# Performance work log

Hardware: AMD Instinct MI355X
Metric: run time of the kernel (lower is better)

Reference implementation:

```python
import jax, jax.numpy as jnp
import numpy as np

DIM = 64
HID = DIM // 8  # 8, hidden width of pos_fc / attn_fc
B, N, V = 1024, 64, 8
NUM_IDS = 10


def setup_inputs() -> dict:
    key = jax.random.key(0)
    ks = jax.random.split(key, 24)
    stdv = 1.0 / np.sqrt(DIM * DIM)
    inp = {
        "q": jax.random.normal(ks[0], (B, N, DIM), jnp.float32),
        "k": jax.random.normal(ks[1], (B, N, V, DIM), jnp.float32),
        "pos": jax.random.normal(ks[2], (B, N, V, 4), jnp.float32),
        "strength": jax.random.normal(ks[3], (512,), jnp.float32),
        # learned params
        "q_tbl": jax.random.uniform(ks[4], (NUM_IDS, DIM * DIM), jnp.float32, -stdv, stdv),
        "k_tbl": jax.random.uniform(ks[5], (NUM_IDS, DIM * DIM), jnp.float32, -stdv, stdv),
        "v_tbl": jax.random.uniform(ks[6], (NUM_IDS, DIM * DIM), jnp.float32, -stdv, stdv),
        "pos_w1": jax.random.normal(ks[7], (4, HID), jnp.float32) * 0.5,
        "pos_b1": jax.random.normal(ks[8], (HID,), jnp.float32) * 0.1,
        "pos_w2": jax.random.normal(ks[9], (HID, DIM), jnp.float32) * 0.2,
        "pos_b2": jax.random.normal(ks[10], (DIM,), jnp.float32) * 0.1,
        "attn_w1": jax.random.normal(ks[11], (DIM, HID), jnp.float32) * 0.1,
        "attn_b1": jax.random.normal(ks[12], (HID,), jnp.float32) * 0.1,
        "attn_w2": jax.random.normal(ks[13], (HID, DIM), jnp.float32) * 0.2,
        "attn_b2": jax.random.normal(ks[14], (DIM,), jnp.float32) * 0.1,
        "out_w": jax.random.normal(ks[15], (DIM, DIM), jnp.float32) * 0.1,
        "out_b": jax.random.normal(ks[16], (DIM,), jnp.float32) * 0.1,
        "str_w": jax.random.normal(ks[17], (512, DIM), jnp.float32) * 0.04,
        "str_b": jax.random.normal(ks[18], (DIM,), jnp.float32) * 0.1,
        # int args
        "mask": jax.random.randint(ks[19], (B, N, V, 1), 0, 2, jnp.int32),
        "embed_id1": 3,
    }
    return inp


def reference(q, k, pos, strength, q_tbl, k_tbl, v_tbl,
              pos_w1, pos_b1, pos_w2, pos_b2,
              attn_w1, attn_b1, attn_w2, attn_b2,
              out_w, out_b, str_w, str_b, mask, embed_id1):
    s = strength @ str_w + str_b                       # [DIM]
    Wq = q_tbl[embed_id1].reshape(DIM, DIM)
    Wk = k_tbl[embed_id1].reshape(DIM, DIM)
    Wv = v_tbl[embed_id1].reshape(DIM, DIM)
    # F.linear(x, W) = x @ W.T ; note v is computed from k (as in source)
    qh = q @ Wq.T + s                                  # [B,N,DIM]
    kh = k @ Wk.T + s                                  # [B,N,V,DIM]
    vh = k @ Wv.T + s                                  # [B,N,V,DIM]
    p = jax.nn.relu(pos @ pos_w1 + pos_b1) @ pos_w2 + pos_b2   # [B,N,V,DIM]
    attn = kh - qh[:, :, None, :] + p                  # [B,N,V,DIM]
    attn = jax.nn.relu(attn @ attn_w1 + attn_b1) @ attn_w2 + attn_b2
    attn = jnp.where(mask == 0, jnp.float32(-1e9), attn)
    attn = jax.nn.softmax(attn, axis=-2)               # softmax over views V
    x = ((vh + p) * attn).sum(axis=2)                  # [B,N,DIM]
    x = x @ out_w + out_b
    return x
```

## Files before the change

kernel.cpp:

```cpp
#include <hip/hip_runtime.h>

#define TBL 4096

#define WS_SPB 0
#define WS_C0  64
#define WS_IMG 128
#define IMG_BH  0
#define IMG_BCT 4
#define IMG_BP  5
#define IMG_BW2 9
#define IMG_BV  13
#define IMG_BO  21

typedef __attribute__((ext_vector_type(8))) short bf16x8;
typedef __attribute__((ext_vector_type(4))) float f32x4;

__device__ inline int cvt2bf(float a, float b) {
    int r;
    asm("v_cvt_pk_bf16_f32 %0, %1, %2" : "=v"(r) : "v"(a), "v"(b));
    return r;
}

__device__ inline bf16x8 pack8(const float* x) {
    union { int4 i; bf16x8 b; } u;
    u.i.x = cvt2bf(x[0], x[1]);
    u.i.y = cvt2bf(x[2], x[3]);
    u.i.z = cvt2bf(x[4], x[5]);
    u.i.w = cvt2bf(x[6], x[7]);
    return u.b;
}

__device__ inline bf16x8 loadpack(const float* p) {
    float4 a = *(const float4*)p;
    float4 b = *(const float4*)(p + 4);
    float t[8] = {a.x, a.y, a.z, a.w, b.x, b.y, b.z, b.w};
    return pack8(t);
}

__device__ inline float swz16(float x) {
    return __int_as_float(__builtin_amdgcn_ds_swizzle(__float_as_int(x), 0x401F));
}

__global__ __launch_bounds__(256) void precompute_kernel(
    const float* __restrict__ strength, const float* __restrict__ str_w,
    const float* __restrict__ str_b,
    const float* __restrict__ q_tbl, const float* __restrict__ k_tbl,
    const float* __restrict__ v_tbl, const float* __restrict__ out_w,
    const float* __restrict__ attn_w1, const float* __restrict__ attn_b1,
    const float* __restrict__ attn_w2,
    const float* __restrict__ pos_w2, const float* __restrict__ pos_b2,
    const int* __restrict__ embed_id, float* __restrict__ ws)
{
    __shared__ float red[4][64];
    __shared__ float red2[4][64][8];

    const int t    = threadIdx.x;
    const int b    = blockIdx.x;
    const int id   = embed_id[0];
    const int lane = t & 63;
    const int dp   = t >> 6;
    const int q4   = lane >> 4;
    const int col  = lane & 15;

    if (b == 0) {
        {
            const float* st = strength + dp * 128;
            const float* sw = str_w + (size_t)(dp * 128) * 64 + lane;
            float a0 = 0.f, a1 = 0.f, a2 = 0.f, a3 = 0.f;
            #pragma unroll
            for (int i = 0; i < 128; i += 4) {
                a0 += st[i]     * sw[(size_t)(i)     * 64];
                a1 += st[i + 1] * sw[(size_t)(i + 1) * 64];
                a2 += st[i + 2] * sw[(size_t)(i + 2) * 64];
                a3 += st[i + 3] * sw[(size_t)(i + 3) * 64];
            }
            red[dp][lane] = (a0 + a1) + (a2 + a3);
        }
        if (t < 8) {
            float c = attn_b1[t];
            #pragma unroll
            for (int d = 0; d < 64; ++d) c += pos_b2[d] * attn_w1[d * 8 + t];
            ws[WS_C0 + t] = c;
        }
        __syncthreads();
        if (t < 64)
            ws[WS_SPB + t] = red[0][t] + red[1][t] + red[2][t] + red[3][t]
                           + str_b[t] + pos_b2[t];
        return;
    }

    const int im = b - 1;

    if (im < 5) {
        float val[8];
        #pragma unroll
        for (int j = 0; j < 8; ++j) val[j] = 0.f;

        if (im < 4) {
            const float* tbl = (im < 2 ? k_tbl : q_tbl) + (size_t)id * TBL;
            const int kb = (im & 1) * 32 + q4 * 8;
            if (col < 8) {
                #pragma unroll
                for (int dd = 0; dd < 16; ++dd) {
                    const int d = dp * 16 + dd;
                    const float w = attn_w1[d * 8 + col];
                    const float4 t0 = *(const float4*)(tbl + d * 64 + kb);
                    const float4 t1 = *(const float4*)(tbl + d * 64 + kb + 4);
                    val[0] += t0.x * w; val[1] += t0.y * w;
                    val[2] += t0.z * w; val[3] += t0.w * w;
                    val[4] += t1.x * w; val[5] += t1.y * w;
                    val[6] += t1.z * w; val[7] += t1.w * w;
                }
            }
        } else {
            if (q4 == 0 && col < 8) {
                #pragma unroll
                for (int dd = 0; dd < 16; ++dd) {
                    const int d = dp * 16 + dd;
                    const float w = attn_w1[d * 8 + col];
                    #pragma unroll
                    for (int j = 0; j < 8; ++j) val[j] += pos_w2[j * 64 + d] * w;
                }
            }
        }
        #pragma unroll
        for (int j = 0; j < 8; ++j) red2[dp][lane][j] = val[j];
        __syncthreads();
        if (dp == 0) {
            const float sgn = (im == 2 || im == 3) ? -1.f : 1.f;
            float v2[8];
            #pragma unroll
            for (int j = 0; j < 8; ++j)
                v2[j] = sgn * (red2[0][lane][j] + red2[1][lane][j] +
                               red2[2][lane][j] + red2[3][lane][j]);
            ((bf16x8*)(ws + WS_IMG))[im * 64 + lane] = pack8(v2);
        }
        return;
    }

    if (dp == 0) {
        float val[8];
        #pragma unroll
        for (int j = 0; j < 8; ++j) val[j] = 0.f;

        if (im < 9) {
            const int tt = im - 5;
            if (q4 == 0) {
                #pragma unroll
                for (int j = 0; j < 8; ++j) val[j] = pos_w2[j * 64 + tt * 16 + col];
            }
        } else if (im < 13) {
            const int tt = im - 9;
            if (q4 == 0) {
                #pragma unroll
                for (int j = 0; j < 8; ++j) val[j] = attn_w2[j * 64 + tt * 16 + col];
            }
        } else if (im < 21) {
            const int e = im - 13, tt = e >> 1, c = e & 1;
            const float* p = v_tbl + (size_t)id * TBL +
                             (tt * 16 + col) * 64 + c * 32 + q4 * 8;
            const float4 t0 = *(const float4*)p;
            const float4 t1 = *(const float4*)(p + 4);
            val[0] = t0.x; val[1] = t0.y; val[2] = t0.z; val[3] = t0.w;
            val[4] = t1.x; val[5] = t1.y; val[6] = t1.z; val[7] = t1.w;
        } else {
            const int e = im - 21, tt = e >> 1, c = e & 1;
            #pragma unroll
            for (int j = 0; j < 8; ++j)
                val[j] = out_w[(c * 32 + q4 * 8 + j) * 64 + tt * 16 + col];
        }
        ((bf16x8*)(ws + WS_IMG))[im * 64 + lane] = pack8(val);
    }
}

__global__ __launch_bounds__(256, 4) void attn2d_main(
    const float* __restrict__ q, const float* __restrict__ k,
    const float* __restrict__ pos,
    const float* __restrict__ pos_w1, const float* __restrict__ pos_b1,
    const float* __restrict__ attn_b2, const float* __restrict__ out_b,
    const int* __restrict__ mask,
    const float* __restrict__ ws, float* __restrict__ out)
{
    __shared__ float rh_lds[4][16 * 12];
    __shared__ float x_lds[4][8 * 68];

    const int tid  = threadIdx.x;
    const int lane = tid & 63;
    const int wiv  = __builtin_amdgcn_readfirstlane(tid >> 6);
    const int q4   = lane >> 4;
    const int col  = lane & 15;

    float* rh_w = rh_lds[wiv];
    float* x_w  = x_lds[wiv];

    const int wid = blockIdx.x * 4 + wiv;
    const bf16x8* img = (const bf16x8*)(ws + WS_IMG);

    bf16x8 Bh[4];
    #pragma unroll
    for (int c = 0; c < 4; ++c) Bh[c] = img[(IMG_BH + c) * 64 + lane];
    const bf16x8 Bct = img[IMG_BCT * 64 + lane];

    float spb[4], b2a[4];
    #pragma unroll
    for (int t = 0; t < 4; ++t) {
        spb[t] = ws[WS_SPB + t * 16 + col];
        b2a[t] = attn_b2[t * 16 + col];
    }
    const float c0r = (col < 8) ? ws[WS_C0 + col] : 0.f;
    const int bnp = q4 >> 1;

    #pragma unroll
    for (int it = 0; it < 4; ++it) {
        const int pair = wid * 4 + it;
        const int bn0  = pair * 2;

        bf16x8 Ak[2], Aq[2];
        #pragma unroll
        for (int c = 0; c < 2; ++c)
            Ak[c] = loadpack(k + ((size_t)pair * 16 + col) * 64 + c * 32 + q4 * 8);
        #pragma unroll
        for (int c = 0; c < 2; ++c)
            Aq[c] = loadpack(q + (size_t)(bn0 + (col >> 3)) * 64 + c * 32 + q4 * 8);

        const int4 m4v = *(const int4*)(mask + (size_t)pair * 16 + q4 * 4);
        const int mm[4] = {m4v.x, m4v.y, m4v.z, m4v.w};

        bf16x8 Ahp{};
        if (lane < 16) {
            float4 pp = *(const float4*)(pos + ((size_t)pair * 16 + lane) * 4);
            float hv[8];
            #pragma unroll
            for (int g = 0; g < 8; ++g)
                hv[g] = fmaxf(pos_b1[g] + pp.x * pos_w1[g] + pp.y * pos_w1[8 + g] +
                              pp.z * pos_w1[16 + g] + pp.w * pos_w1[24 + g], 0.f);
            Ahp = pack8(hv);
        }

        f32x4 acch = {0.f, 0.f, 0.f, 0.f};
        acch = __builtin_amdgcn_mfma_f32_16x16x32_bf16(Ak[0], Bh[0], acch, 0, 0, 0);
        acch = __builtin_amdgcn_mfma_f32_16x16x32_bf16(Ak[1], Bh[1], acch, 0, 0, 0);
        acch = __builtin_amdgcn_mfma_f32_16x16x32_bf16(Aq[0], Bh[2], acch, 0, 0, 0);
        acch = __builtin_amdgcn_mfma_f32_16x16x32_bf16(Aq[1], Bh[3], acch, 0, 0, 0);
        acch = __builtin_amdgcn_mfma_f32_16x16x32_bf16(Ahp,   Bct,   acch, 0, 0, 0);
        if (col < 8) {
            #pragma unroll
            for (int r = 0; r < 4; ++r)
                rh_w[(q4 * 4 + r) * 12 + col] = fmaxf(acch[r] + c0r, 0.f);
        }

        bf16x8 Arh{};
        if (q4 == 0) {
            float4 a  = *(const float4*)&rh_w[col * 12];
            float4 bb = *(const float4*)&rh_w[col * 12 + 4];
            float rr[8] = {a.x, a.y, a.z, a.w, bb.x, bb.y, bb.z, bb.w};
            Arh = pack8(rr);
        }

        #pragma unroll
        for (int t = 0; t < 4; ++t) {
            const bf16x8 Bv0 = img[(IMG_BV + t * 2) * 64 + lane];
            const bf16x8 Bv1 = img[(IMG_BV + t * 2 + 1) * 64 + lane];
            const bf16x8 Bp  = img[(IMG_BP + t) * 64 + lane];
            const bf16x8 Bw  = img[(IMG_BW2 + t) * 64 + lane];

            f32x4 vh = {0.f, 0.f, 0.f, 0.f};
            vh = __builtin_amdgcn_mfma_f32_16x16x32_bf16(Ak[0], Bv0, vh, 0, 0, 0);
            vh = __builtin_amdgcn_mfma_f32_16x16x32_bf16(Ak[1], Bv1, vh, 0, 0, 0);
            vh = __builtin_amdgcn_mfma_f32_16x16x32_bf16(Ahp,   Bp,  vh, 0, 0, 0);
            f32x4 at = {0.f, 0.f, 0.f, 0.f};
            at = __builtin_amdgcn_mfma_f32_16x16x32_bf16(Arh, Bw, at, 0, 0, 0);

            float lg[4];
            #pragma unroll
            for (int r = 0; r < 4; ++r)
                lg[r] = (mm[r] != 0) ? (at[r] + b2a[t]) : -1e9f;

            float mx = fmaxf(fmaxf(lg[0], lg[1]), fmaxf(lg[2], lg[3]));
            mx = fmaxf(mx, swz16(mx));
            float wsum = 0.f, xp = 0.f;
            #pragma unroll
            for (int r = 0; r < 4; ++r) {
                const float wv = __expf(lg[r] - mx);
                wsum += wv;
                xp   += wv * (vh[r] + spb[t]);
            }
            wsum += swz16(wsum);
            xp   += swz16(xp);
            const float xv = xp * __builtin_amdgcn_rcpf(wsum);
            if ((q4 & 1) == 0)
                x_w[(it * 2 + bnp) * 68 + t * 16 + col] = xv;
        }
    }

    bf16x8 Ax[2];
    #pragma unroll
    for (int c = 0; c < 2; ++c)
        Ax[c] = loadpack(&x_w[(col & 7) * 68 + c * 32 + q4 * 8]);
    #pragma unroll
    for (int t = 0; t < 4; ++t) {
        const bf16x8 Bo0 = img[(IMG_BO + t * 2) * 64 + lane];
        const bf16x8 Bo1 = img[(IMG_BO + t * 2 + 1) * 64 + lane];
        f32x4 a = {0.f, 0.f, 0.f, 0.f};
        a = __builtin_amdgcn_mfma_f32_16x16x32_bf16(Ax[0], Bo0, a, 0, 0, 0);
        a = __builtin_amdgcn_mfma_f32_16x16x32_bf16(Ax[1], Bo1, a, 0, 0, 0);
        const float ob = out_b[t * 16 + col];
        #pragma unroll
        for (int r = 0; r < 4; ++r) {
            const int row = q4 * 4 + r;
            if (row < 8)
                out[((size_t)wid * 8 + row) * 64 + t * 16 + col] = a[r] + ob;
        }
    }
}

extern "C" void kernel_launch(void* const* d_in, const int* in_sizes, int n_in,
                              void* d_out, int out_size, void* d_ws, size_t ws_size,
                              hipStream_t stream) {
    const float* q        = (const float*)d_in[0];
    const float* k        = (const float*)d_in[1];
    const float* pos      = (const float*)d_in[2];
    const float* strength = (const float*)d_in[3];
    const float* q_tbl    = (const float*)d_in[4];
    const float* k_tbl    = (const float*)d_in[5];
    const float* v_tbl    = (const float*)d_in[6];
    const float* pos_w1   = (const float*)d_in[7];
    const float* pos_b1   = (const float*)d_in[8];
    const float* pos_w2   = (const float*)d_in[9];
    const float* pos_b2   = (const float*)d_in[10];
    const float* attn_w1  = (const float*)d_in[11];
    const float* attn_b1  = (const float*)d_in[12];
    const float* attn_w2  = (const float*)d_in[13];
    const float* attn_b2  = (const float*)d_in[14];
    const float* out_w    = (const float*)d_in[15];
    const float* out_b    = (const float*)d_in[16];
    const float* str_w    = (const float*)d_in[17];
    const float* str_b    = (const float*)d_in[18];
    const int*   mask     = (const int*)d_in[19];
    const int*   embed    = (const int*)d_in[20];
    float* ws  = (float*)d_ws;
    float* out = (float*)d_out;

    hipLaunchKernelGGL(precompute_kernel, dim3(30), dim3(256), 0, stream,
                       strength, str_w, str_b, q_tbl, k_tbl, v_tbl, out_w,
                       attn_w1, attn_b1, attn_w2, pos_w2, pos_b2, embed, ws);
    hipLaunchKernelGGL(attn2d_main, dim3(2048), dim3(256), 0, stream,
                       q, k, pos, pos_w1, pos_b1, attn_b2, out_b, mask, ws, out);
}
```

Before: 270.2 us.

## Software-pipeline k/q/pos/mask loads and hoist weight fragments into registers

Prefetches the raw k, q, pos and mask data for the next pair while the current pair's MFMAs and softmax run, double-buffering them in registers. The per-tile B-fragment loads for V, pos, attn_w2 and out_w are hoisted out of the inner loops into registers. Launch bounds drop from 4 to 3 waves-per-EU occupancy to make room for the extra registers. This is meant to hide global memory latency, at the cost of lower occupancy.

```diff
diff --git a/kernel.cpp b/kernel.cpp
--- a/kernel.cpp
+++ b/kernel.cpp
@@ -30,11 +30,15 @@
     return u.b;
 }
 
+__device__ inline bf16x8 pack2f4(float4 a, float4 b) {
+    float t[8] = {a.x, a.y, a.z, a.w, b.x, b.y, b.z, b.w};
+    return pack8(t);
+}
+
 __device__ inline bf16x8 loadpack(const float* p) {
     float4 a = *(const float4*)p;
     float4 b = *(const float4*)(p + 4);
-    float t[8] = {a.x, a.y, a.z, a.w, b.x, b.y, b.z, b.w};
-    return pack8(t);
+    return pack2f4(a, b);
 }
 
 __device__ inline float swz16(float x) {
@@ -173,7 +177,7 @@
     }
 }
 
-__global__ __launch_bounds__(256, 4) void attn2d_main(
+__global__ __launch_bounds__(256, 3) void attn2d_main(
     const float* __restrict__ q, const float* __restrict__ k,
     const float* __restrict__ pos,
     const float* __restrict__ pos_w1, const float* __restrict__ pos_b1,
@@ -200,6 +204,14 @@
     #pragma unroll
     for (int c = 0; c < 4; ++c) Bh[c] = img[(IMG_BH + c) * 64 + lane];
     const bf16x8 Bct = img[IMG_BCT * 64 + lane];
+    bf16x8 Bv[4][2], Bp[4], Bw[4];
+    #pragma unroll
+    for (int t = 0; t < 4; ++t) {
+        Bv[t][0] = img[(IMG_BV + t * 2) * 64 + lane];
+        Bv[t][1] = img[(IMG_BV + t * 2 + 1) * 64 + lane];
+        Bp[t]    = img[(IMG_BP + t) * 64 + lane];
+        Bw[t]    = img[(IMG_BW2 + t) * 64 + lane];
+    }
 
     float spb[4], b2a[4];
     #pragma unroll
@@ -210,32 +222,50 @@
     const float c0r = (col < 8) ? ws[WS_C0 + col] : 0.f;
     const int bnp = q4 >> 1;
 
+#define LOADRAW(PAIR, RK, RQ, RP, RM) do {                                    \
+        const size_t kb_ = ((size_t)(PAIR) * 16 + col) * 64 + q4 * 8;         \
+        RK[0] = *(const float4*)(k + kb_);                                    \
+        RK[1] = *(const float4*)(k + kb_ + 4);                                \
+        RK[2] = *(const float4*)(k + kb_ + 32);                               \
+        RK[3] = *(const float4*)(k + kb_ + 36);                               \
+        const size_t qb_ = ((size_t)(PAIR) * 2 + (col >> 3)) * 64 + q4 * 8;   \
+        RQ[0] = *(const float4*)(q + qb_);                                    \
+        RQ[1] = *(const float4*)(q + qb_ + 4);                                \
+        RQ[2] = *(const float4*)(q + qb_ + 32);                               \
+        RQ[3] = *(const float4*)(q + qb_ + 36);                               \
+        if (lane < 16)                                                        \
+            RP = *(const float4*)(pos + ((size_t)(PAIR) * 16 + lane) * 4);    \
+        RM = *(const int4*)(mask + (size_t)(PAIR) * 16 + q4 * 4);             \
+    } while (0)
+
+    float4 rk[4], rq[4], rp = make_float4(0.f, 0.f, 0.f, 0.f);
+    int4   rm = make_int4(1, 1, 1, 1);
+    LOADRAW(wid * 4, rk, rq, rp, rm);
+
     #pragma unroll
     for (int it = 0; it < 4; ++it) {
         const int pair = wid * 4 + it;
-        const int bn0  = pair * 2;
 
         bf16x8 Ak[2], Aq[2];
-        #pragma unroll
-        for (int c = 0; c < 2; ++c)
-            Ak[c] = loadpack(k + ((size_t)pair * 16 + col) * 64 + c * 32 + q4 * 8);
-        #pragma unroll
-        for (int c = 0; c < 2; ++c)
-            Aq[c] = loadpack(q + (size_t)(bn0 + (col >> 3)) * 64 + c * 32 + q4 * 8);
-
-        const int4 m4v = *(const int4*)(mask + (size_t)pair * 16 + q4 * 4);
-        const int mm[4] = {m4v.x, m4v.y, m4v.z, m4v.w};
+        Ak[0] = pack2f4(rk[0], rk[1]);
+        Ak[1] = pack2f4(rk[2], rk[3]);
+        Aq[0] = pack2f4(rq[0], rq[1]);
+        Aq[1] = pack2f4(rq[2], rq[3]);
+        const int mm[4] = {rm.x, rm.y, rm.z, rm.w};
 
         bf16x8 Ahp{};
         if (lane < 16) {
-            float4 pp = *(const float4*)(pos + ((size_t)pair * 16 + lane) * 4);
             float hv[8];
             #pragma unroll
             for (int g = 0; g < 8; ++g)
-                hv[g] = fmaxf(pos_b1[g] + pp.x * pos_w1[g] + pp.y * pos_w1[8 + g] +
-                              pp.z * pos_w1[16 + g] + pp.w * pos_w1[24 + g], 0.f);
+                hv[g] = fmaxf(pos_b1[g] + rp.x * pos_w1[g] + rp.y * pos_w1[8 + g] +
+                              rp.z * pos_w1[16 + g] + rp.w * pos_w1[24 + g], 0.f);
             Ahp = pack8(hv);
         }
+
+        float4 nk[4], nq[4], np = make_float4(0.f, 0.f, 0.f, 0.f);
+        int4   nm = make_int4(1, 1, 1, 1);
+        if (it < 3) LOADRAW(pair + 1, nk, nq, np, nm);
 
         f32x4 acch = {0.f, 0.f, 0.f, 0.f};
         acch = __builtin_amdgcn_mfma_f32_16x16x32_bf16(Ak[0], Bh[0], acch, 0, 0, 0);
@@ -253,23 +283,17 @@
         if (q4 == 0) {
             float4 a  = *(const float4*)&rh_w[col * 12];
             float4 bb = *(const float4*)&rh_w[col * 12 + 4];
-            float rr[8] = {a.x, a.y, a.z, a.w, bb.x, bb.y, bb.z, bb.w};
-            Arh = pack8(rr);
+            Arh = pack2f4(a, bb);
         }
 
         #pragma unroll
         for (int t = 0; t < 4; ++t) {
-            const bf16x8 Bv0 = img[(IMG_BV + t * 2) * 64 + lane];
-            const bf16x8 Bv1 = img[(IMG_BV + t * 2 + 1) * 64 + lane];
-            const bf16x8 Bp  = img[(IMG_BP + t) * 64 + lane];
-            const bf16x8 Bw  = img[(IMG_BW2 + t) * 64 + lane];
-
             f32x4 vh = {0.f, 0.f, 0.f, 0.f};
-            vh = __builtin_amdgcn_mfma_f32_16x16x32_bf16(Ak[0], Bv0, vh, 0, 0, 0);
-            vh = __builtin_amdgcn_mfma_f32_16x16x32_bf16(Ak[1], Bv1, vh, 0, 0, 0);
-            vh = __builtin_amdgcn_mfma_f32_16x16x32_bf16(Ahp,   Bp,  vh, 0, 0, 0);
+            vh = __builtin_amdgcn_mfma_f32_16x16x32_bf16(Ak[0], Bv[t][0], vh, 0, 0, 0);
+            vh = __builtin_amdgcn_mfma_f32_16x16x32_bf16(Ak[1], Bv[t][1], vh, 0, 0, 0);
+            vh = __builtin_amdgcn_mfma_f32_16x16x32_bf16(Ahp,   Bp[t],    vh, 0, 0, 0);
             f32x4 at = {0.f, 0.f, 0.f, 0.f};
-            at = __builtin_amdgcn_mfma_f32_16x16x32_bf16(Arh, Bw, at, 0, 0, 0);
+            at = __builtin_amdgcn_mfma_f32_16x16x32_bf16(Arh, Bw[t], at, 0, 0, 0);
 
             float lg[4];
             #pragma unroll
@@ -291,19 +315,30 @@
             if ((q4 & 1) == 0)
                 x_w[(it * 2 + bnp) * 68 + t * 16 + col] = xv;
         }
-    }
+
+        if (it < 3) {
+            #pragma unroll
+            for (int c = 0; c < 4; ++c) { rk[c] = nk[c]; rq[c] = nq[c]; }
+            rp = np; rm = nm;
+        }
+    }
+#undef LOADRAW
 
     bf16x8 Ax[2];
     #pragma unroll
     for (int c = 0; c < 2; ++c)
         Ax[c] = loadpack(&x_w[(col & 7) * 68 + c * 32 + q4 * 8]);
+    bf16x8 Bo[4][2];
     #pragma unroll
     for (int t = 0; t < 4; ++t) {
-        const bf16x8 Bo0 = img[(IMG_BO + t * 2) * 64 + lane];
-        const bf16x8 Bo1 = img[(IMG_BO + t * 2 + 1) * 64 + lane];
+        Bo[t][0] = img[(IMG_BO + t * 2) * 64 + lane];
+        Bo[t][1] = img[(IMG_BO + t * 2 + 1) * 64 + lane];
+    }
+    #pragma unroll
+    for (int t = 0; t < 4; ++t) {
         f32x4 a = {0.f, 0.f, 0.f, 0.f};
-        a = __builtin_amdgcn_mfma_f32_16x16x32_bf16(Ax[0], Bo0, a, 0, 0, 0);
-        a = __builtin_amdgcn_mfma_f32_16x16x32_bf16(Ax[1], Bo1, a, 0, 0, 0);
+        a = __builtin_amdgcn_mfma_f32_16x16x32_bf16(Ax[0], Bo[t][0], a, 0, 0, 0);
+        a = __builtin_amdgcn_mfma_f32_16x16x32_bf16(Ax[1], Bo[t][1], a, 0, 0, 0);
         const float ob = out_b[t * 16 + col];
         #pragma unroll
         for (int r = 0; r < 4; ++r) {
```

Measured after the change: 285.5 us. 1.06x slower.
